# Optimization experiments

Hardware: AMD Instinct MI355X
Metric: run time of the kernel (lower is better)

## Reference

```python
import jax, jax.numpy as jnp
import numpy as np

DEPTH_CHANNEL = 48  # max_disp(192) / downsample_scale(4)


def setup_inputs() -> dict:
    key = jax.random.key(0)
    k1, k2 = jax.random.split(key)
    B, C, H, W = 4, 512, 96, 312
    left_features = jax.random.normal(k1, (B, C, H, W), dtype=jnp.float32)
    right_features = jax.random.normal(k2, (B, C, H, W), dtype=jnp.float32)
    return {"left_features": left_features, "right_features": right_features}


def reference(left_features, right_features):
    # PSM cosine cost volume: for each disparity i,
    #   cost[:, i, :, i:] = mean_c(left[:, :, :, i:] * right[:, :, :, :W-i])
    # positions w < i remain zero (from the pre-zeroed tensor in the original).
    B, C, H, W = left_features.shape
    planes = []
    for i in range(DEPTH_CHANNEL):  # small fixed disparity loop (48), unrolled under jit
        corr = jnp.mean(
            left_features[:, :, :, i:] * right_features[:, :, :, : W - i],
            axis=1,
        )  # [B, H, W-i]
        planes.append(jnp.pad(corr, ((0, 0), (0, 0), (i, 0))))  # zero-fill w < i
    return jnp.stack(planes, axis=1)  # [B, D, H, W]
```

## Files before the change

### kernel.cpp

```cpp
#include <hip/hip_runtime.h>
#include <hip/hip_bf16.h>
#include <stdint.h>


#define B_ 4
#define C_ 512
#define H_ 96
#define W_ 312
#define D_ 48
#define HW_ (H_ * W_)
#define CHW_ (C_ * HW_)

#define KC 64
#define NCHUNK (C_ / KC)
#define NQ 4
#define QW 80
#define LCOLS 80
#define RCOLS 128
#define PITCH 128
#define LBYTES (LCOLS * PITCH)
#define RBYTES (RCOLS * PITCH)
#define SMEM_BYTES (LBYTES + RBYTES)

#define THREADS 256
#define LITEMS 3
#define RITEMS 4

typedef __bf16 bf16x8 __attribute__((ext_vector_type(8)));
typedef float  f32x4  __attribute__((ext_vector_type(4)));

__device__ __forceinline__ uint32_t pack2_bf16(float a, float b) {
    uint32_t r;
    asm("v_cvt_pk_bf16_f32 %0, %1, %2" : "=v"(r) : "v"(a), "v"(b));
    return r;
}

__device__ __forceinline__ int lds_slotoff(int lw, int chi) {
    return lw * PITCH + ((chi ^ (lw & 7) ^ ((lw >> 4) & 7)) << 4);
}

__device__ __forceinline__ void lds_barrier() {
    asm volatile("s_waitcnt lgkmcnt(0)" ::: "memory");
    __builtin_amdgcn_s_barrier();
}

__global__ __launch_bounds__(THREADS, 2)
void psm_cost_volume(const float* __restrict__ lf,
                     const float* __restrict__ rf,
                     float* __restrict__ out) {
    const int wq   = blockIdx.x * QW;
    const int h    = blockIdx.y;
    const int b    = blockIdx.z;
    const int tid  = threadIdx.x;
    const int lane = tid & 63;
    const int wave = tid >> 6;
    const int l15  = lane & 15;
    const int l4   = lane >> 4;
    const int jj   = wave;

    extern __shared__ char smem[];

    const float* lbase = lf + (size_t)b * CHW_ + (size_t)h * W_;
    const float* rbase = rf + (size_t)b * CHW_ + (size_t)h * W_;

    f32x4 acc[5];
    #pragma unroll
    for (int i = 0; i < 5; ++i) acc[i] = f32x4{0.f, 0.f, 0.f, 0.f};

    f32x4 pl0[LITEMS], pl1[LITEMS], pr0[RITEMS], pr1[RITEMS];

    auto LOADS = [&](int c0) {
        #pragma unroll
        for (int it = 0; it < LITEMS; ++it) {
            int idx = tid + it * THREADS;
            if (idx < 32 * 20) {
                int rp = idx / 20;
                int q  = idx - rp * 20;
                int w4 = wq + 4 * q;
                pl0[it] = f32x4{0.f, 0.f, 0.f, 0.f};
                pl1[it] = f32x4{0.f, 0.f, 0.f, 0.f};
                if (w4 + 3 < W_) {
                    const float* g = lbase + (size_t)(c0 + 2 * rp) * HW_ + w4;
                    pl0[it] = *(const f32x4*)g;
                    pl1[it] = *(const f32x4*)(g + HW_);
                }
            }
        }
        #pragma unroll
        for (int it = 0; it < RITEMS; ++it) {
            int idx = tid + it * THREADS;
            int rp  = idx >> 5;
            int q   = idx & 31;
            int w4  = wq - 48 + 4 * q;
            pr0[it] = f32x4{0.f, 0.f, 0.f, 0.f};
            pr1[it] = f32x4{0.f, 0.f, 0.f, 0.f};
            if (w4 >= 0 && w4 + 3 < W_) {
                const float* g = rbase + (size_t)(c0 + 2 * rp) * HW_ + w4;
                pr0[it] = *(const f32x4*)g;
                pr1[it] = *(const f32x4*)(g + HW_);
            }
        }
    };

    auto WRITES = [&]() {
        #pragma unroll
        for (int it = 0; it < LITEMS; ++it) {
            int idx = tid + it * THREADS;
            if (idx < 32 * 20) {
                int rp  = idx / 20;
                int q   = idx - rp * 20;
                int chi = rp >> 2;
                int cb  = (rp & 3) << 2;
                #pragma unroll
                for (int j = 0; j < 4; ++j) {
                    int lw = 4 * q + j;
                    *(uint32_t*)(smem + lds_slotoff(lw, chi) + cb) =
                        pack2_bf16(pl0[it][j], pl1[it][j]);
                }
            }
        }
        #pragma unroll
        for (int it = 0; it < RITEMS; ++it) {
            int idx = tid + it * THREADS;
            int rp  = idx >> 5;
            int q   = idx & 31;
            int chi = rp >> 2;
            int cb  = (rp & 3) << 2;
            #pragma unroll
            for (int j = 0; j < 4; ++j) {
                int lw = 4 * q + j;
                *(uint32_t*)(smem + LBYTES + lds_slotoff(lw, chi) + cb) =
                    pack2_bf16(pr0[it][j], pr1[it][j]);
            }
        }
    };

    LOADS(0);
    for (int ch = 0; ch < NCHUNK; ++ch) {
        if (ch) lds_barrier();
        WRITES();
        if (ch + 1 < NCHUNK) LOADS((ch + 1) * KC);
        lds_barrier();

        #pragma unroll
        for (int ks = 0; ks < 2; ++ks) {
            const int chi = ks * 4 + l4;
            #pragma unroll
            for (int pi = 0; pi < 5; ++pi) {
                const int lwB = 16 * pi + l15;
                const int lwA = 16 * (pi + jj) + l15;
                bf16x8 bfrag = *(const bf16x8*)(smem + lds_slotoff(lwB, chi));
                bf16x8 afrag = *(const bf16x8*)(smem + LBYTES + lds_slotoff(lwA, chi));
                acc[pi] = __builtin_amdgcn_mfma_f32_16x16x32_bf16(afrag, bfrag, acc[pi], 0, 0, 0);
            }
        }
    }
    __syncthreads();

    float* outs = (float*)smem;
    #pragma unroll
    for (int pi = 0; pi < 5; ++pi) {
        const int lw = 16 * pi + l15;
        #pragma unroll
        for (int r = 0; r < 4; ++r) {
            int tm = 4 * l4 + r;
            int d  = 48 - 16 * jj + l15 - tm;
            if (d >= 0 && d < D_) {
                outs[d * QW + lw] = acc[pi][r] * (1.f / 512.f);
            }
        }
    }
    __syncthreads();

    float* obase = out + (size_t)b * (D_ * HW_) + (size_t)h * W_ + wq;
    #pragma unroll
    for (int it = 0; it < (D_ * QW) / THREADS; ++it) {
        int idx = it * THREADS + tid;
        int d   = idx / QW;
        int lw  = idx - d * QW;
        if (wq + lw < W_) {
            obase[(size_t)d * HW_ + lw] = outs[idx];
        }
    }
}

extern "C" void kernel_launch(void* const* d_in, const int* in_sizes, int n_in,
                              void* d_out, int out_size, void* d_ws, size_t ws_size,
                              hipStream_t stream) {
    const float* lf = (const float*)d_in[0];
    const float* rf = (const float*)d_in[1];
    float* out = (float*)d_out;
    dim3 grid(NQ, H_, B_);
    psm_cost_volume<<<grid, THREADS, SMEM_BYTES, stream>>>(lf, rf, out);
}
```

Measured before the change: 122.6 us.

## Double-buffer LDS chunks and swizzle workgroup order across a flattened grid

```diff
diff --git a/kernel.cpp b/kernel.cpp
--- a/kernel.cpp
+++ b/kernel.cpp
@@ -20,9 +20,11 @@
 #define PITCH 128
 #define LBYTES (LCOLS * PITCH)
 #define RBYTES (RCOLS * PITCH)
-#define SMEM_BYTES (LBYTES + RBYTES)
+#define SMEM_HALF (LBYTES + RBYTES)
+#define SMEM_BYTES (2 * SMEM_HALF)
 
 #define THREADS 256
+#define NWG (NQ * H_ * B_)
 #define LITEMS 3
 #define RITEMS 4
 
@@ -48,9 +50,14 @@
 void psm_cost_volume(const float* __restrict__ lf,
                      const float* __restrict__ rf,
                      float* __restrict__ out) {
-    const int wq   = blockIdx.x * QW;
-    const int h    = blockIdx.y;
-    const int b    = blockIdx.z;
+    const int lid = blockIdx.x;
+    const int swz = (lid & 7) * (NWG / 8) + (lid >> 3);
+    const int q   = swz & 3;
+    const int t   = swz >> 2;
+    const int b   = t / H_;
+    const int h   = t - b * H_;
+    const int wq  = q * QW;
+
     const int tid  = threadIdx.x;
     const int lane = tid & 63;
     const int wave = tid >> 6;
@@ -75,8 +82,8 @@
             int idx = tid + it * THREADS;
             if (idx < 32 * 20) {
                 int rp = idx / 20;
-                int q  = idx - rp * 20;
-                int w4 = wq + 4 * q;
+                int q4 = idx - rp * 20;
+                int w4 = wq + 4 * q4;
                 pl0[it] = f32x4{0.f, 0.f, 0.f, 0.f};
                 pl1[it] = f32x4{0.f, 0.f, 0.f, 0.f};
                 if (w4 + 3 < W_) {
@@ -90,8 +97,8 @@
         for (int it = 0; it < RITEMS; ++it) {
             int idx = tid + it * THREADS;
             int rp  = idx >> 5;
-            int q   = idx & 31;
-            int w4  = wq - 48 + 4 * q;
+            int q4  = idx & 31;
+            int w4  = wq - 48 + 4 * q4;
             pr0[it] = f32x4{0.f, 0.f, 0.f, 0.f};
             pr1[it] = f32x4{0.f, 0.f, 0.f, 0.f};
             if (w4 >= 0 && w4 + 3 < W_) {
@@ -102,19 +109,19 @@
         }
     };
 
-    auto WRITES = [&]() {
+    auto WRITES = [&](char* buf) {
         #pragma unroll
         for (int it = 0; it < LITEMS; ++it) {
             int idx = tid + it * THREADS;
             if (idx < 32 * 20) {
                 int rp  = idx / 20;
-                int q   = idx - rp * 20;
+                int q4  = idx - rp * 20;
                 int chi = rp >> 2;
                 int cb  = (rp & 3) << 2;
                 #pragma unroll
                 for (int j = 0; j < 4; ++j) {
-                    int lw = 4 * q + j;
-                    *(uint32_t*)(smem + lds_slotoff(lw, chi) + cb) =
+                    int lw = 4 * q4 + j;
+                    *(uint32_t*)(buf + lds_slotoff(lw, chi) + cb) =
                         pack2_bf16(pl0[it][j], pl1[it][j]);
                 }
             }
@@ -123,24 +130,26 @@
         for (int it = 0; it < RITEMS; ++it) {
             int idx = tid + it * THREADS;
             int rp  = idx >> 5;
-            int q   = idx & 31;
+            int q4  = idx & 31;
             int chi = rp >> 2;
             int cb  = (rp & 3) << 2;
             #pragma unroll
             for (int j = 0; j < 4; ++j) {
-                int lw = 4 * q + j;
-                *(uint32_t*)(smem + LBYTES + lds_slotoff(lw, chi) + cb) =
+                int lw = 4 * q4 + j;
+                *(uint32_t*)(buf + LBYTES + lds_slotoff(lw, chi) + cb) =
                     pack2_bf16(pr0[it][j], pr1[it][j]);
             }
         }
     };
 
     LOADS(0);
+    WRITES(smem);
+    LOADS(KC);
+    lds_barrier();
+
     for (int ch = 0; ch < NCHUNK; ++ch) {
-        if (ch) lds_barrier();
-        WRITES();
-        if (ch + 1 < NCHUNK) LOADS((ch + 1) * KC);
-        lds_barrier();
+        const int cur = ch & 1;
+        const char* rdbuf = smem + cur * SMEM_HALF;
 
         #pragma unroll
         for (int ks = 0; ks < 2; ++ks) {
@@ -149,10 +158,16 @@
             for (int pi = 0; pi < 5; ++pi) {
                 const int lwB = 16 * pi + l15;
                 const int lwA = 16 * (pi + jj) + l15;
-                bf16x8 bfrag = *(const bf16x8*)(smem + lds_slotoff(lwB, chi));
-                bf16x8 afrag = *(const bf16x8*)(smem + LBYTES + lds_slotoff(lwA, chi));
+                bf16x8 bfrag = *(const bf16x8*)(rdbuf + lds_slotoff(lwB, chi));
+                bf16x8 afrag = *(const bf16x8*)(rdbuf + LBYTES + lds_slotoff(lwA, chi));
                 acc[pi] = __builtin_amdgcn_mfma_f32_16x16x32_bf16(afrag, bfrag, acc[pi], 0, 0, 0);
             }
+        }
+
+        if (ch + 1 < NCHUNK) {
+            WRITES(smem + (cur ^ 1) * SMEM_HALF);
+            if (ch + 2 < NCHUNK) LOADS((ch + 2) * KC);
+            lds_barrier();
         }
     }
     __syncthreads();
@@ -190,6 +205,5 @@
     const float* lf = (const float*)d_in[0];
     const float* rf = (const float*)d_in[1];
     float* out = (float*)d_out;
-    dim3 grid(NQ, H_, B_);
-    psm_cost_volume<<<grid, THREADS, SMEM_BYTES, stream>>>(lf, rf, out);
-}
+    psm_cost_volume<<<dim3(NWG), THREADS, SMEM_BYTES, stream>>>(lf, rf, out);
+}
```

New measurement: 111.9 us. 1.1x faster.
